# Kernel optimization log

Measured on AMD Instinct MI355X. Metric: run time of the kernel, lower is better.

The kernel has to match this reference:

```python
import jax, jax.numpy as jnp
import numpy as np

IN_F = 4096
OUT_F = 4096
BATCH = 8192


def setup_inputs() -> dict:
    key = jax.random.key(0)
    ks = jax.random.split(key, 7)
    # Xavier-normal-ish mu, rho = -3 as in reset_parameters (plus small noise for generality)
    xav = float(np.sqrt(2.0 / (IN_F + OUT_F)))
    return {
        "x": jax.random.normal(ks[0], (BATCH, IN_F), jnp.float32),
        "weight_mu": jax.random.normal(ks[1], (OUT_F, IN_F), jnp.float32) * xav,
        "weight_rho": jnp.full((OUT_F, IN_F), -3.0, jnp.float32)
        + 0.1 * jax.random.normal(ks[2], (OUT_F, IN_F), jnp.float32),
        "bias_mu": jnp.zeros((OUT_F,), jnp.float32),
        "bias_rho": jnp.full((OUT_F,), -3.0, jnp.float32)
        + 0.1 * jax.random.normal(ks[3], (OUT_F,), jnp.float32),
        "weight_eps": jax.random.normal(ks[4], (OUT_F, IN_F), jnp.float32),
        "bias_eps": jax.random.normal(ks[5], (OUT_F,), jnp.float32),
    }


def reference(x, weight_mu, weight_rho, bias_mu, bias_rho, weight_eps, bias_eps):
    # sigma = log1p(exp(rho)) = softplus(rho); sampled weight = mu + sigma * eps
    weight = weight_mu + jax.nn.softplus(weight_rho) * weight_eps  # [out, in]
    bias = bias_mu + jax.nn.softplus(bias_rho) * bias_eps          # [out]
    # F.linear: x @ weight.T + bias
    return jnp.einsum("bi,oi->bo", x, weight) + bias
```

## Files before the change

kernel.cpp:

```cpp
#include <hip/hip_runtime.h>
#include <hip/hip_bf16.h>
#include <math.h>

typedef __bf16 bf16;
typedef __attribute__((ext_vector_type(8))) __bf16 bf16x8;
typedef __attribute__((ext_vector_type(4))) float f32x4;

typedef const uint32_t __attribute__((address_space(1)))* gp1_t;
typedef uint32_t __attribute__((address_space(3)))* lp3_t;

__device__ __forceinline__ void async_load16(const void* g, void* l) {
    __builtin_amdgcn_global_load_lds((gp1_t)g, (lp3_t)l, 16, 0, 0);
}

__device__ __forceinline__ float softplus_f(float x) {
    return fmaxf(x, 0.0f) + log1pf(__expf(-fabsf(x)));
}

#define IN_F  4096
#define OUT_F 4096
#define BATCH 8192

#define BM 128
#define BN 128

#define NXB ((BATCH * IN_F) / (256 * 8))
#define NWB ((OUT_F * IN_F) / (256 * 8))

__global__ __launch_bounds__(256) void prologue(
    const float* __restrict__ x,
    const float* __restrict__ mu, const float* __restrict__ rho,
    const float* __restrict__ eps,
    bf16* __restrict__ xb, bf16* __restrict__ W)
{
    const int b = blockIdx.x;
    if (b < NXB) {
        const int i = (b * 256 + threadIdx.x) * 8;
        float4 a = *(const float4*)(x + i);
        float4 c = *(const float4*)(x + i + 4);
        bf16x8 o;
        o[0] = (bf16)a.x; o[1] = (bf16)a.y; o[2] = (bf16)a.z; o[3] = (bf16)a.w;
        o[4] = (bf16)c.x; o[5] = (bf16)c.y; o[6] = (bf16)c.z; o[7] = (bf16)c.w;
        *(bf16x8*)(xb + i) = o;
    } else {
        const int i = ((b - NXB) * 256 + threadIdx.x) * 8;
        bf16x8 w;
#pragma unroll
        for (int h = 0; h < 2; ++h) {
            float4 m = *(const float4*)(mu + i + h * 4);
            float4 r = *(const float4*)(rho + i + h * 4);
            float4 e = *(const float4*)(eps + i + h * 4);
            w[h * 4 + 0] = (bf16)(m.x + softplus_f(r.x) * e.x);
            w[h * 4 + 1] = (bf16)(m.y + softplus_f(r.y) * e.y);
            w[h * 4 + 2] = (bf16)(m.z + softplus_f(r.z) * e.z);
            w[h * 4 + 3] = (bf16)(m.w + softplus_f(r.w) * e.w);
        }
        *(bf16x8*)(W + i) = w;
    }
}

__global__ __launch_bounds__(256, 3) void gemm_bt_bias(
    const bf16* __restrict__ A,
    const bf16* __restrict__ W,
    const float* __restrict__ bmu, const float* __restrict__ brho,
    const float* __restrict__ beps,
    float* __restrict__ C)
{
    const int K = IN_F;
    const int N = OUT_F;

    __shared__ __align__(16) bf16 As[2][BM * 32];
    __shared__ __align__(16) bf16 Bs[2][BN * 32];

    const int tid  = threadIdx.x;
    const int wave = tid >> 6;
    const int lane = tid & 63;

    const int bn = blockIdx.x & 31;
    const int bm = blockIdx.x >> 5;
    const int row0 = bm * BM;
    const int col0 = bn * BN;

    const int wm   = (wave >> 1) * 64;
    const int wn   = (wave & 1) * 64;
    const int l15  = lane & 15;
    const int quad = lane >> 4;

    const f32x4 zero = {0.f, 0.f, 0.f, 0.f};
    f32x4 acc[4][4];
#pragma unroll
    for (int i = 0; i < 4; ++i)
#pragma unroll
        for (int j = 0; j < 4; ++j) acc[i][j] = zero;

    const int srow = tid >> 2;
    const int scol = (tid & 3) << 3;
    const bf16* gA0 = A + (size_t)(row0 + srow) * K + scol;
    const bf16* gA1 = gA0 + (size_t)64 * K;
    const bf16* gB0 = W + (size_t)(col0 + srow) * K + scol;
    const bf16* gB1 = gB0 + (size_t)64 * K;

    char* const ldsA = (char*)As + wave * 1024;
    char* const ldsB = (char*)Bs + wave * 1024;

    for (int k0 = 0; k0 < K; k0 += 64) {
        async_load16(gA0 + k0,      ldsA);
        async_load16(gA1 + k0,      ldsA + 4096);
        async_load16(gA0 + k0 + 32, ldsA + 8192);
        async_load16(gA1 + k0 + 32, ldsA + 12288);
        async_load16(gB0 + k0,      ldsB);
        async_load16(gB1 + k0,      ldsB + 4096);
        async_load16(gB0 + k0 + 32, ldsB + 8192);
        async_load16(gB1 + k0 + 32, ldsB + 12288);
        __syncthreads();

#pragma unroll
        for (int h = 0; h < 2; ++h) {
            bf16x8 a[4], b[4];
#pragma unroll
            for (int mt = 0; mt < 4; ++mt)
                a[mt] = *(const bf16x8*)&As[h][(wm + mt * 16 + l15) * 32 + quad * 8];
#pragma unroll
            for (int nt = 0; nt < 4; ++nt)
                b[nt] = *(const bf16x8*)&Bs[h][(wn + nt * 16 + l15) * 32 + quad * 8];

#pragma unroll
            for (int mt = 0; mt < 4; ++mt)
#pragma unroll
                for (int nt = 0; nt < 4; ++nt)
                    acc[mt][nt] = __builtin_amdgcn_mfma_f32_16x16x32_bf16(
                        a[mt], b[nt], acc[mt][nt], 0, 0, 0);
        }

        __syncthreads();
    }

    float bias[4];
#pragma unroll
    for (int nt = 0; nt < 4; ++nt) {
        const int col = col0 + wn + nt * 16 + l15;
        bias[nt] = bmu[col] + softplus_f(brho[col]) * beps[col];
    }

#pragma unroll
    for (int mt = 0; mt < 4; ++mt) {
#pragma unroll
        for (int r = 0; r < 4; ++r) {
            const size_t row = row0 + wm + mt * 16 + quad * 4 + r;
#pragma unroll
            for (int nt = 0; nt < 4; ++nt) {
                const int col = col0 + wn + nt * 16 + l15;
                C[row * N + col] = acc[mt][nt][r] + bias[nt];
            }
        }
    }
}

extern "C" void kernel_launch(void* const* d_in, const int* in_sizes, int n_in,
                              void* d_out, int out_size, void* d_ws, size_t ws_size,
                              hipStream_t stream) {
    const float* x    = (const float*)d_in[0];
    const float* wmu  = (const float*)d_in[1];
    const float* wrho = (const float*)d_in[2];
    const float* bmu  = (const float*)d_in[3];
    const float* brho = (const float*)d_in[4];
    const float* weps = (const float*)d_in[5];
    const float* beps = (const float*)d_in[6];
    float* out = (float*)d_out;

    bf16* xb = (bf16*)d_ws;
    bf16* W  = (bf16*)((char*)d_ws + (size_t)BATCH * IN_F * sizeof(bf16));

    prologue<<<NXB + NWB, 256, 0, stream>>>(x, wmu, wrho, weps, xb, W);

    gemm_bt_bias<<<(BATCH / BM) * (OUT_F / BN), 256, 0, stream>>>(
        xb, W, bmu, brho, beps, out);
}
```

Before: 642.4 us.

## Rewrite GEMM as 256x256 tile, 8-wave pingpong pipeline with swizzled LDS

Raises the block tile to 256x256 with 512 threads. The K loop becomes a double-buffered, quarter-staged async-load pipeline with XOR-swizzled LDS layout, barrier-interleaved MFMA phases and setprio. The goal is to overlap global loads with MFMA work, cut LDS bank conflicts and raise data reuse per block. The softplus now uses a fast log in place of log1pf, which is slightly less accurate; the larger tile also costs registers and occupancy.

```diff
diff --git a/kernel.cpp b/kernel.cpp
--- a/kernel.cpp
+++ b/kernel.cpp
@@ -14,15 +14,15 @@
 }
 
 __device__ __forceinline__ float softplus_f(float x) {
-    return fmaxf(x, 0.0f) + log1pf(__expf(-fabsf(x)));
+    return fmaxf(x, 0.0f) + __logf(1.0f + __expf(-fabsf(x)));
 }
 
 #define IN_F  4096
 #define OUT_F 4096
 #define BATCH 8192
 
-#define BM 128
-#define BN 128
+#define BM 256
+#define BN 256
 
 #define NXB ((BATCH * IN_F) / (256 * 8))
 #define NWB ((OUT_F * IN_F) / (256 * 8))
@@ -59,101 +59,164 @@
     }
 }
 
-__global__ __launch_bounds__(256, 3) void gemm_bt_bias(
+__global__ __launch_bounds__(512, 2) void gemm_bt_bias(
     const bf16* __restrict__ A,
     const bf16* __restrict__ W,
     const float* __restrict__ bmu, const float* __restrict__ brho,
     const float* __restrict__ beps,
     float* __restrict__ C)
 {
-    const int K = IN_F;
-    const int N = OUT_F;
-
-    __shared__ __align__(16) bf16 As[2][BM * 32];
-    __shared__ __align__(16) bf16 Bs[2][BN * 32];
+    __shared__ __align__(16) bf16 lds[2][2][2][128 * 64];
 
     const int tid  = threadIdx.x;
-    const int wave = tid >> 6;
     const int lane = tid & 63;
-
-    const int bn = blockIdx.x & 31;
-    const int bm = blockIdx.x >> 5;
+    const int l15  = lane & 15;
+    const int quad = lane >> 4;
+
+    const int bn = blockIdx.x & 15;
+    const int bm = blockIdx.x >> 4;
     const int row0 = bm * BM;
     const int col0 = bn * BN;
 
-    const int wm   = (wave >> 1) * 64;
-    const int wn   = (wave & 1) * 64;
-    const int l15  = lane & 15;
-    const int quad = lane >> 4;
+    const int wave = tid >> 6;
+    const int wmh = wave >> 2;
+    const int wnq = wave & 3;
+    const int wbh = wnq >> 1;
+    const int nb  = (wnq & 1) * 64;
 
     const f32x4 zero = {0.f, 0.f, 0.f, 0.f};
-    f32x4 acc[4][4];
-#pragma unroll
-    for (int i = 0; i < 4; ++i)
-#pragma unroll
-        for (int j = 0; j < 4; ++j) acc[i][j] = zero;
-
-    const int srow = tid >> 2;
-    const int scol = (tid & 3) << 3;
-    const bf16* gA0 = A + (size_t)(row0 + srow) * K + scol;
-    const bf16* gA1 = gA0 + (size_t)64 * K;
-    const bf16* gB0 = W + (size_t)(col0 + srow) * K + scol;
-    const bf16* gB1 = gB0 + (size_t)64 * K;
-
-    char* const ldsA = (char*)As + wave * 1024;
-    char* const ldsB = (char*)Bs + wave * 1024;
-
-    for (int k0 = 0; k0 < K; k0 += 64) {
-        async_load16(gA0 + k0,      ldsA);
-        async_load16(gA1 + k0,      ldsA + 4096);
-        async_load16(gA0 + k0 + 32, ldsA + 8192);
-        async_load16(gA1 + k0 + 32, ldsA + 12288);
-        async_load16(gB0 + k0,      ldsB);
-        async_load16(gB1 + k0,      ldsB + 4096);
-        async_load16(gB0 + k0 + 32, ldsB + 8192);
-        async_load16(gB1 + k0 + 32, ldsB + 12288);
-        __syncthreads();
-
+    f32x4 acc[8][4];
+#pragma unroll
+    for (int i2 = 0; i2 < 8; ++i2)
+#pragma unroll
+        for (int j2 = 0; j2 < 4; ++j2) acc[i2][j2] = zero;
+
+    const int ldsw = (tid & ~63) * 16;
+
+    auto STAGE = [&](int m, int t) {
+        const int buf = t & 1;
+        const int k0  = (t < (IN_F / 64) ? t : (IN_F / 64 - 1)) << 6;
+        const bf16* g = (m < 2) ? A : W;
+        const int gr  = ((m < 2) ? row0 : col0) + ((m & 1) << 7);
+        char* slot = (char*)&lds[buf][m >> 1][m & 1][0];
+#pragma unroll
+        for (int j = 0; j < 2; ++j) {
+            const int p    = j * 8192 + tid * 16;
+            const int r    = p >> 7;
+            const int irow = (p & 127) ^ ((r & 7) << 4);
+            async_load16(g + (size_t)(gr + r) * IN_F + k0 + (irow >> 1),
+                         slot + j * 8192 + ldsw);
+        }
+    };
+
+#define FRAG(SLOT, ROW, KQ)                                                  \
+    (*(const bf16x8*)((SLOT) + (ROW) * 128 +                                 \
+                      (((KQ) * 64 + quad * 16) ^ (((ROW) & 7) << 4))))
+
+#define MFMA_Q(AF, BF, MB, NB_)                                              \
+    {                                                                        \
+        _Pragma("unroll")                                                    \
+        for (int kq = 0; kq < 2; ++kq)                                       \
+            _Pragma("unroll")                                                \
+            for (int f = 0; f < 4; ++f)                                      \
+                _Pragma("unroll")                                            \
+                for (int g2 = 0; g2 < 2; ++g2)                               \
+                    acc[(MB) + f][(NB_) + g2] =                              \
+                        __builtin_amdgcn_mfma_f32_16x16x32_bf16(             \
+                            AF[f][kq], BF[g2][kq],                           \
+                            acc[(MB) + f][(NB_) + g2], 0, 0, 0);             \
+    }
+
+    STAGE(0, 0); STAGE(1, 0); STAGE(2, 0); STAGE(3, 0);
+    STAGE(0, 1); STAGE(1, 1);
+    asm volatile("s_waitcnt vmcnt(4)" ::: "memory");
+    asm volatile("s_barrier" ::: "memory");
+
+    bf16x8 a0[4][2], a1[4][2], b0[2][2], b1[2][2];
+
+    for (int i = 0; i < IN_F / 128; ++i) {
 #pragma unroll
         for (int h = 0; h < 2; ++h) {
-            bf16x8 a[4], b[4];
-#pragma unroll
-            for (int mt = 0; mt < 4; ++mt)
-                a[mt] = *(const bf16x8*)&As[h][(wm + mt * 16 + l15) * 32 + quad * 8];
-#pragma unroll
-            for (int nt = 0; nt < 4; ++nt)
-                b[nt] = *(const bf16x8*)&Bs[h][(wn + nt * 16 + l15) * 32 + quad * 8];
-
-#pragma unroll
-            for (int mt = 0; mt < 4; ++mt)
-#pragma unroll
-                for (int nt = 0; nt < 4; ++nt)
-                    acc[mt][nt] = __builtin_amdgcn_mfma_f32_16x16x32_bf16(
-                        a[mt], b[nt], acc[mt][nt], 0, 0, 0);
-        }
-
-        __syncthreads();
+            const int tc = 2 * i + h;
+            const char* SA = (const char*)&lds[h][0][wmh][0];
+            const char* SB = (const char*)&lds[h][1][wbh][0];
+
+#pragma unroll
+            for (int f = 0; f < 4; ++f) {
+                a0[f][0] = FRAG(SA, f * 16 + l15, 0);
+                a0[f][1] = FRAG(SA, f * 16 + l15, 1);
+            }
+#pragma unroll
+            for (int f = 0; f < 2; ++f) {
+                b0[f][0] = FRAG(SB, nb + f * 16 + l15, 0);
+                b0[f][1] = FRAG(SB, nb + f * 16 + l15, 1);
+            }
+            STAGE(2, tc + 1);
+            asm volatile("s_barrier" ::: "memory");
+            asm volatile("s_waitcnt lgkmcnt(0)" ::: "memory");
+            __builtin_amdgcn_sched_barrier(0);
+            __builtin_amdgcn_s_setprio(1);
+            MFMA_Q(a0, b0, 0, 0);
+            __builtin_amdgcn_s_setprio(0);
+            asm volatile("s_barrier" ::: "memory");
+
+#pragma unroll
+            for (int f = 0; f < 4; ++f) {
+                a1[f][0] = FRAG(SA, 64 + f * 16 + l15, 0);
+                a1[f][1] = FRAG(SA, 64 + f * 16 + l15, 1);
+            }
+#pragma unroll
+            for (int f = 0; f < 2; ++f) {
+                b1[f][0] = FRAG(SB, nb + 32 + f * 16 + l15, 0);
+                b1[f][1] = FRAG(SB, nb + 32 + f * 16 + l15, 1);
+            }
+            STAGE(3, tc + 1);
+            asm volatile("s_barrier" ::: "memory");
+            asm volatile("s_waitcnt lgkmcnt(0)" ::: "memory");
+            __builtin_amdgcn_sched_barrier(0);
+            __builtin_amdgcn_s_setprio(1);
+            MFMA_Q(a0, b1, 0, 2);
+            __builtin_amdgcn_s_setprio(0);
+            asm volatile("s_barrier" ::: "memory");
+
+            STAGE(0, tc + 2);
+            asm volatile("s_barrier" ::: "memory");
+            __builtin_amdgcn_s_setprio(1);
+            MFMA_Q(a1, b0, 4, 0);
+            __builtin_amdgcn_s_setprio(0);
+            asm volatile("s_barrier" ::: "memory");
+
+            STAGE(1, tc + 2);
+            asm volatile("s_barrier" ::: "memory");
+            __builtin_amdgcn_s_setprio(1);
+            MFMA_Q(a1, b1, 4, 2);
+            __builtin_amdgcn_s_setprio(0);
+            asm volatile("s_waitcnt vmcnt(4)" ::: "memory");
+            asm volatile("s_barrier" ::: "memory");
+        }
     }
 
     float bias[4];
 #pragma unroll
-    for (int nt = 0; nt < 4; ++nt) {
-        const int col = col0 + wn + nt * 16 + l15;
-        bias[nt] = bmu[col] + softplus_f(brho[col]) * beps[col];
-    }
-
-#pragma unroll
-    for (int mt = 0; mt < 4; ++mt) {
+    for (int f = 0; f < 4; ++f) {
+        const int col = col0 + wnq * 64 + f * 16 + l15;
+        bias[f] = bmu[col] + softplus_f(brho[col]) * beps[col];
+    }
+
+#pragma unroll
+    for (int mf = 0; mf < 8; ++mf) {
 #pragma unroll
         for (int r = 0; r < 4; ++r) {
-            const size_t row = row0 + wm + mt * 16 + quad * 4 + r;
-#pragma unroll
-            for (int nt = 0; nt < 4; ++nt) {
-                const int col = col0 + wn + nt * 16 + l15;
-                C[row * N + col] = acc[mt][nt][r] + bias[nt];
-            }
-        }
-    }
+            const size_t row = (size_t)row0 + wmh * 128 + mf * 16 + quad * 4 + r;
+#pragma unroll
+            for (int f = 0; f < 4; ++f) {
+                const int col = col0 + wnq * 64 + f * 16 + l15;
+                C[row * OUT_F + col] = acc[mf][f][r] + bias[f];
+            }
+        }
+    }
+#undef FRAG
+#undef MFMA_Q
 }
 
 extern "C" void kernel_launch(void* const* d_in, const int* in_sizes, int n_in,
@@ -173,6 +236,6 @@
 
     prologue<<<NXB + NWB, 256, 0, stream>>>(x, wmu, wrho, weps, xb, W);
 
-    gemm_bt_bias<<<(BATCH / BM) * (OUT_F / BN), 256, 0, stream>>>(
+    gemm_bt_bias<<<(BATCH / BM) * (OUT_F / BN), 512, 0, stream>>>(
         xb, W, bmu, brho, beps, out);
 }
```

Result: slower. 663.0 us (+3.2%).
